# Optimization experiments

Hardware: AMD Instinct MI355X
Metric: run time of the kernel (lower is better)

## Reference

```python
import jax, jax.numpy as jnp
import numpy as np

DIM = 768
NUM_HEADS = 12
SCALE = 1.0 / (DIM ** 0.5)  # NOTE: source scales by 1/sqrt(dim), not 1/sqrt(head_dim)


def setup_inputs() -> dict:
    key = jax.random.key(0)
    k_x, k_qkv, k_ow, k_ob = jax.random.split(key, 4)
    b, n = 8, 1024
    x = jax.random.normal(k_x, (b, n, DIM), dtype=jnp.float32)
    # torch Linear weight is [out, in]; we store jax-style [in, out]
    w_qkv = jax.random.normal(k_qkv, (DIM, 3 * DIM), dtype=jnp.float32) * (DIM ** -0.5)
    w_out = jax.random.normal(k_ow, (DIM, DIM), dtype=jnp.float32) * (DIM ** -0.5)
    b_out = jax.random.normal(k_ob, (DIM,), dtype=jnp.float32) * 0.01
    return {"x": x, "w_qkv": w_qkv, "w_out": w_out, "b_out": b_out}


def reference(x, w_qkv, w_out, b_out):
    b, n, c = x.shape
    h = NUM_HEADS
    hd = c // h
    qkv = (x @ w_qkv).reshape(b, n, 3, h, hd)
    q, k, v = jnp.moveaxis(qkv, 2, 0)          # each [b, n, h, hd]
    q = jnp.swapaxes(q, 1, 2)                  # [b, h, n, hd]
    k = jnp.swapaxes(k, 1, 2)
    v = jnp.swapaxes(v, 1, 2)
    dot = jnp.einsum('bhqd,bhkd->bhqk', q, k) * SCALE
    attn = jax.nn.softmax(dot, axis=-1)        # attn_dropout p=0 -> identity
    out = jnp.einsum('bhqk,bhkd->bhqd', attn, v)
    out = jnp.swapaxes(out, 1, 2).reshape(b, n, c)
    return out @ w_out + b_out                 # proj_dropout p=0 -> identity
```

## Files before the change

### kernel.cpp

```cpp
#include <hip/hip_runtime.h>

#define DEV __device__ __forceinline__

typedef __bf16 bf16x8 __attribute__((ext_vector_type(8)));
typedef float  f32x4  __attribute__((ext_vector_type(4)));
typedef float  f32x16 __attribute__((ext_vector_type(16)));
typedef unsigned int u32x4 __attribute__((ext_vector_type(4)));

static constexpr float SCALE = 0.036084391824351615f;
static constexpr float L2E   = 1.4426950408889634f;

DEV unsigned short f2bf(float f) {
  return __builtin_bit_cast(unsigned short, (__bf16)f);
}
DEV unsigned int pack2(float a, float b) {
  return (unsigned int)f2bf(a) | ((unsigned int)f2bf(b) << 16);
}

#define GLDS16(gp, lp) \
  __builtin_amdgcn_global_load_lds((__attribute__((address_space(1))) void*)(gp), \
                                   (__attribute__((address_space(3))) void*)(lp), 16, 0, 0)


__global__ __launch_bounds__(256) void k_cvt_bf16(const float* __restrict__ in,
                                                  unsigned short* __restrict__ out,
                                                  int n8) {
  int i = blockIdx.x * 256 + threadIdx.x;
  if (i >= n8) return;
  const float4* p = (const float4*)in + (size_t)i * 2;
  float4 a = p[0], b = p[1];
  uint4 r;
  r.x = pack2(a.x, a.y); r.y = pack2(a.z, a.w);
  r.z = pack2(b.x, b.y); r.w = pack2(b.z, b.w);
  ((uint4*)out)[i] = r;
}

__global__ __launch_bounds__(256) void k_transpose_w(const float* __restrict__ in,
                                                     unsigned short* __restrict__ out,
                                                     int R, int C) {
  __shared__ float tile[64][65];
  int c0 = blockIdx.x * 64, r0 = blockIdx.y * 64;
  int t = threadIdx.x, tr = t >> 6, tc = t & 63;
#pragma unroll
  for (int i = 0; i < 64; i += 4)
    tile[i + tr][tc] = in[(size_t)(r0 + i + tr) * C + c0 + tc];
  __syncthreads();
#pragma unroll
  for (int i = 0; i < 64; i += 4)
    out[(size_t)(c0 + i + tr) * R + r0 + tc] = f2bf(tile[tc][i + tr]);
}

template <int MODE>
__global__ __launch_bounds__(256) void k_gemm(const unsigned short* __restrict__ A,
                                              const unsigned short* __restrict__ BT,
                                              void* __restrict__ out0,
                                              unsigned short* __restrict__ Kb,
                                              unsigned short* __restrict__ VTb,
                                              const float* __restrict__ bias) {
  __shared__ __align__(16) char smem[32768];
  char* As = smem;
  char* Bs = smem + 16384;
  const int tid = threadIdx.x;
  const int wave = tid >> 6, lane = tid & 63;
  const int g = lane >> 4, l15 = lane & 15;
  const int wrow = wave >> 1, wcol = wave & 1;

  int id = blockIdx.y * gridDim.x + blockIdx.x;
  int per_xcd = (gridDim.x * gridDim.y) >> 3;
  int id2 = (id & 7) * per_xcd + (id >> 3);
  const int bm = id2 / gridDim.x, bn = id2 % gridDim.x;

  f32x4 acc[4][4] = {};
  const unsigned short* Abase = A + (size_t)bm * 128 * 768;
  const unsigned short* Bbase = BT + (size_t)bn * 128 * 768;

  for (int kt = 0; kt < 12; ++kt) {
    const int k0 = kt * 64;
#pragma unroll
    for (int i = 0; i < 4; ++i) {
      int q = i * 256 + tid;
      int row = q >> 3, c = q & 7;
      int cs = c ^ (row & 7);
      GLDS16(Abase + (size_t)row * 768 + k0 + cs * 8, As + (i * 256 + wave * 64) * 16);
      GLDS16(Bbase + (size_t)row * 768 + k0 + cs * 8, Bs + (i * 256 + wave * 64) * 16);
    }
    __syncthreads();
    __builtin_amdgcn_s_setprio(1);
#pragma unroll
    for (int kk = 0; kk < 2; ++kk) {
      bf16x8 af[4], bfr[4];
#pragma unroll
      for (int mi = 0; mi < 4; ++mi) {
        int r = wrow * 64 + mi * 16 + l15;
        af[mi] = *(const bf16x8*)(As + r * 128 + (((kk * 4 + g) ^ (r & 7)) * 16));
      }
#pragma unroll
      for (int ni = 0; ni < 4; ++ni) {
        int r = wcol * 64 + ni * 16 + l15;
        bfr[ni] = *(const bf16x8*)(Bs + r * 128 + (((kk * 4 + g) ^ (r & 7)) * 16));
      }
#pragma unroll
      for (int mi = 0; mi < 4; ++mi)
#pragma unroll
        for (int ni = 0; ni < 4; ++ni)
          acc[mi][ni] = __builtin_amdgcn_mfma_f32_16x16x32_bf16(af[mi], bfr[ni], acc[mi][ni], 0, 0, 0);
    }
    __builtin_amdgcn_s_setprio(0);
    __syncthreads();
  }

  const int row0 = bm * 128 + wrow * 64;
  const int col0 = bn * 128 + wcol * 64;
#pragma unroll
  for (int mi = 0; mi < 4; ++mi) {
#pragma unroll
    for (int ni = 0; ni < 4; ++ni) {
      int col = col0 + ni * 16 + l15;
      if (MODE == 0) {
        int which = col / 768;
        int hd = col - which * 768;
        int head = hd >> 6, d = hd & 63;
        int rowm0 = row0 + mi * 16 + g * 4;
        int bi = rowm0 >> 10, np = rowm0 & 1023;
        if (which == 0) {
#pragma unroll
          for (int j = 0; j < 4; ++j)
            ((unsigned short*)out0)[((size_t)(bi * 12 + head) * 1024 + np + j) * 64 + d] =
                f2bf(acc[mi][ni][j] * (SCALE * L2E));
        } else if (which == 1) {
#pragma unroll
          for (int j = 0; j < 4; ++j)
            Kb[((size_t)(bi * 12 + head) * 1024 + np + j) * 64 + d] = f2bf(acc[mi][ni][j]);
        } else {
          ushort4 w;
          w.x = f2bf(acc[mi][ni][0]); w.y = f2bf(acc[mi][ni][1]);
          w.z = f2bf(acc[mi][ni][2]); w.w = f2bf(acc[mi][ni][3]);
          *(ushort4*)(VTb + ((size_t)(bi * 12 + head) * 64 + d) * 1024 + np) = w;
        }
      } else {
        float bz = bias[col];
#pragma unroll
        for (int j = 0; j < 4; ++j) {
          int rowm = row0 + mi * 16 + g * 4 + j;
          ((float*)out0)[(size_t)rowm * 768 + col] = acc[mi][ni][j] + bz;
        }
      }
    }
  }
}

__global__ __launch_bounds__(256) void k_attn(const unsigned short* __restrict__ Qb,
                                              const unsigned short* __restrict__ Kb,
                                              const unsigned short* __restrict__ VTb,
                                              unsigned short* __restrict__ Ao) {
  __shared__ __align__(16) char smem[32768];
  const int tid = threadIdx.x, wave = tid >> 6, lane = tid & 63;
  const int hi = lane >> 5, q31 = lane & 31;
  const int bh = blockIdx.x % 96, qt = blockIdx.x / 96;
  const int qbase = qt * 128 + wave * 32;
  const unsigned short* Kp = Kb + (size_t)bh * 65536;
  const unsigned short* Vp = VTb + (size_t)bh * 65536;

  auto STAGE = [&](int buf, int kt) {
#pragma unroll
    for (int i = 0; i < 2; ++i) {
      int c = i * 4 + wave;
      GLDS16(Kp + (size_t)(kt * 64 + lane) * 64 + c * 8,
             smem + buf * 8192 + (i * 256 + wave * 64) * 16);
      GLDS16(Vp + (size_t)lane * 1024 + kt * 64 + c * 8,
             smem + 16384 + buf * 8192 + (i * 256 + wave * 64) * 16);
    }
  };

  bf16x8 aq[4];
#pragma unroll
  for (int dk = 0; dk < 4; ++dk)
    aq[dk] = *(const bf16x8*)(Qb + (size_t)bh * 65536 +
                              (size_t)(qbase + q31) * 64 + dk * 16 + hi * 8);

  bf16x8 vones;
#pragma unroll
  for (int e = 0; e < 8; ++e) vones[e] = (__bf16)1.0f;

  f32x16 o0 = {}, o1 = {};
  f32x16 lacc = {};

  STAGE(0, 0);
  __syncthreads();
  int cur = 0;

  for (int kt = 0; kt < 16; ++kt) {
    if (kt < 15) STAGE(cur ^ 1, kt + 1);
    char* Ks = smem + cur * 8192;
    char* Vs = smem + 16384 + cur * 8192;

#pragma unroll
    for (int sub = 0; sub < 2; ++sub) {
      f32x16 st = {};
      __builtin_amdgcn_s_setprio(1);
#pragma unroll
      for (int dk = 0; dk < 4; ++dk) {
        bf16x8 ka = *(const bf16x8*)(Ks + (((dk * 2 + hi) * 64 + sub * 32 + q31) * 16));
        st = __builtin_amdgcn_mfma_f32_32x32x16_bf16(ka, aq[dk], st, 0, 0, 0);
      }
      __builtin_amdgcn_s_setprio(0);

      float ex[16];
#pragma unroll
      for (int r2 = 0; r2 < 16; ++r2) ex[r2] = __builtin_amdgcn_exp2f(st[r2]);

      unsigned w00 = pack2(ex[0], ex[1]),   w01 = pack2(ex[2], ex[3]);
      unsigned w10 = pack2(ex[4], ex[5]),   w11 = pack2(ex[6], ex[7]);
      unsigned w20 = pack2(ex[8], ex[9]),   w21 = pack2(ex[10], ex[11]);
      unsigned w30 = pack2(ex[12], ex[13]), w31 = pack2(ex[14], ex[15]);

      auto pA = __builtin_amdgcn_permlane32_swap(w00, w10, false, false);
      auto pB = __builtin_amdgcn_permlane32_swap(w01, w11, false, false);
      auto pC = __builtin_amdgcn_permlane32_swap(w20, w30, false, false);
      auto pD = __builtin_amdgcn_permlane32_swap(w21, w31, false, false);

      __builtin_amdgcn_s_setprio(1);
#pragma unroll
      for (int s = 0; s < 2; ++s) {
        u32x4 au;
        if (s == 0) { au[0] = pA[0]; au[1] = pB[0]; au[2] = pA[1]; au[3] = pB[1]; }
        else        { au[0] = pC[0]; au[1] = pD[0]; au[2] = pC[1]; au[3] = pD[1]; }
        bf16x8 pa = __builtin_bit_cast(bf16x8, au);
        int ch = sub * 4 + s * 2 + hi;
        bf16x8 vb0 = *(const bf16x8*)(Vs + (ch * 64 + q31) * 16);
        bf16x8 vb1 = *(const bf16x8*)(Vs + (ch * 64 + 32 + q31) * 16);
        o0   = __builtin_amdgcn_mfma_f32_32x32x16_bf16(pa, vb0, o0, 0, 0, 0);
        o1   = __builtin_amdgcn_mfma_f32_32x32x16_bf16(pa, vb1, o1, 0, 0, 0);
        lacc = __builtin_amdgcn_mfma_f32_32x32x16_bf16(pa, vones, lacc, 0, 0, 0);
      }
      __builtin_amdgcn_s_setprio(0);
    }

    __syncthreads();
    cur ^= 1;
  }

  const int b_idx = bh / 12, h = bh - b_idx * 12;
#pragma unroll
  for (int m = 0; m < 4; ++m) {
#pragma unroll
    for (int j = 0; j < 4; ++j) {
      int reg = m * 4 + j;
      int qr = j + 8 * m + 4 * hi;
      float linv = 1.0f / lacc[reg];
      size_t base = (size_t)(b_idx * 1024 + qbase + qr) * 768 + h * 64 + q31;
      Ao[base]      = f2bf(o0[reg] * linv);
      Ao[base + 32] = f2bf(o1[reg] * linv);
    }
  }
}


extern "C" void kernel_launch(void* const* d_in, const int* in_sizes, int n_in,
                              void* d_out, int out_size, void* d_ws, size_t ws_size,
                              hipStream_t stream) {
  const float* x     = (const float*)d_in[0];
  const float* w_qkv = (const float*)d_in[1];
  const float* w_out = (const float*)d_in[2];
  const float* b_out = (const float*)d_in[3];

  char* ws = (char*)d_ws;
  size_t off = 0;
  auto alloc = [&](size_t bytes) {
    void* p = ws + off;
    off += (bytes + 255) & ~(size_t)255;
    return p;
  };
  unsigned short* xb    = (unsigned short*)alloc(8192ull * 768 * 2);
  unsigned short* wqkvT = (unsigned short*)alloc(2304ull * 768 * 2);
  unsigned short* woutT = (unsigned short*)alloc(768ull * 768 * 2);
  unsigned short* Qb    = (unsigned short*)alloc(96ull * 1024 * 64 * 2);
  unsigned short* Kbf   = (unsigned short*)alloc(96ull * 1024 * 64 * 2);
  unsigned short* VTb   = (unsigned short*)alloc(96ull * 1024 * 64 * 2);
  unsigned short* Aob   = (unsigned short*)alloc(96ull * 1024 * 64 * 2);

  k_cvt_bf16<<<3072, 256, 0, stream>>>(x, xb, 786432);
  k_transpose_w<<<dim3(36, 12), 256, 0, stream>>>(w_qkv, wqkvT, 768, 2304);
  k_transpose_w<<<dim3(12, 12), 256, 0, stream>>>(w_out, woutT, 768, 768);
  k_gemm<0><<<dim3(18, 64), 256, 0, stream>>>(xb, wqkvT, Qb, Kbf, VTb, nullptr);
  k_attn<<<768, 256, 0, stream>>>(Qb, Kbf, VTb, Aob);
  k_gemm<1><<<dim3(6, 64), 256, 0, stream>>>(Aob, woutT, d_out, nullptr, nullptr, b_out);
}
```

Measured before the change: 110.4 us.

## Merge prep kernels into one launch and interleave QK MFMA sub-tiles in attention

Folds the x bf16 conversion and both weight transposes into a single k_prep launch, saving two kernel launches and their gaps. In the attention kernel, both 32-key QK^T score tiles are now computed together before the softmax/PV loop, so two independent MFMA chains can interleave. It also adds a minimum-occupancy hint of 3 blocks per CU via launch_bounds. The hint and the extra live accumulator registers may force spills or lower occupancy.

```diff
diff --git a/kernel.cpp b/kernel.cpp
--- a/kernel.cpp
+++ b/kernel.cpp
@@ -21,26 +21,36 @@
   __builtin_amdgcn_global_load_lds((__attribute__((address_space(1))) void*)(gp), \
                                    (__attribute__((address_space(3))) void*)(lp), 16, 0, 0)
 
-
-__global__ __launch_bounds__(256) void k_cvt_bf16(const float* __restrict__ in,
-                                                  unsigned short* __restrict__ out,
-                                                  int n8) {
-  int i = blockIdx.x * 256 + threadIdx.x;
-  if (i >= n8) return;
-  const float4* p = (const float4*)in + (size_t)i * 2;
-  float4 a = p[0], b = p[1];
-  uint4 r;
-  r.x = pack2(a.x, a.y); r.y = pack2(a.z, a.w);
-  r.z = pack2(b.x, b.y); r.w = pack2(b.z, b.w);
-  ((uint4*)out)[i] = r;
-}
-
-__global__ __launch_bounds__(256) void k_transpose_w(const float* __restrict__ in,
-                                                     unsigned short* __restrict__ out,
-                                                     int R, int C) {
+__global__ __launch_bounds__(256) void k_prep(const float* __restrict__ x,
+                                              const float* __restrict__ w_qkv,
+                                              const float* __restrict__ w_out,
+                                              unsigned short* __restrict__ xb,
+                                              unsigned short* __restrict__ wqkvT,
+                                              unsigned short* __restrict__ woutT) {
   __shared__ float tile[64][65];
-  int c0 = blockIdx.x * 64, r0 = blockIdx.y * 64;
-  int t = threadIdx.x, tr = t >> 6, tc = t & 63;
+  int b = blockIdx.x, t = threadIdx.x;
+  if (b < 3072) {
+    int i = b * 256 + t;
+    const float4* p = (const float4*)x + (size_t)i * 2;
+    float4 a = p[0], bb = p[1];
+    uint4 r;
+    r.x = pack2(a.x, a.y); r.y = pack2(a.z, a.w);
+    r.z = pack2(bb.x, bb.y); r.w = pack2(bb.z, bb.w);
+    ((uint4*)xb)[i] = r;
+    return;
+  }
+  const float* in;
+  unsigned short* out;
+  int R, C, bx, by;
+  if (b < 3504) {
+    int tt = b - 3072; in = w_qkv; out = wqkvT; R = 768; C = 2304;
+    bx = tt % 36; by = tt / 36;
+  } else {
+    int tt = b - 3504; in = w_out; out = woutT; R = 768; C = 768;
+    bx = tt % 12; by = tt / 12;
+  }
+  int c0 = bx * 64, r0 = by * 64;
+  int tr = t >> 6, tc = t & 63;
 #pragma unroll
   for (int i = 0; i < 64; i += 4)
     tile[i + tr][tc] = in[(size_t)(r0 + i + tr) * C + c0 + tc];
@@ -149,10 +159,10 @@
   }
 }
 
-__global__ __launch_bounds__(256) void k_attn(const unsigned short* __restrict__ Qb,
-                                              const unsigned short* __restrict__ Kb,
-                                              const unsigned short* __restrict__ VTb,
-                                              unsigned short* __restrict__ Ao) {
+__global__ __launch_bounds__(256, 3) void k_attn(const unsigned short* __restrict__ Qb,
+                                                 const unsigned short* __restrict__ Kb,
+                                                 const unsigned short* __restrict__ VTb,
+                                                 unsigned short* __restrict__ Ao) {
   __shared__ __align__(16) char smem[32768];
   const int tid = threadIdx.x, wave = tid >> 6, lane = tid & 63;
   const int hi = lane >> 5, q31 = lane & 31;
@@ -194,17 +204,20 @@
     char* Ks = smem + cur * 8192;
     char* Vs = smem + 16384 + cur * 8192;
 
+    f32x16 st0 = {}, st1 = {};
+    __builtin_amdgcn_s_setprio(1);
+#pragma unroll
+    for (int dk = 0; dk < 4; ++dk) {
+      bf16x8 ka0 = *(const bf16x8*)(Ks + (((dk * 2 + hi) * 64 + q31) * 16));
+      bf16x8 ka1 = *(const bf16x8*)(Ks + (((dk * 2 + hi) * 64 + 32 + q31) * 16));
+      st0 = __builtin_amdgcn_mfma_f32_32x32x16_bf16(ka0, aq[dk], st0, 0, 0, 0);
+      st1 = __builtin_amdgcn_mfma_f32_32x32x16_bf16(ka1, aq[dk], st1, 0, 0, 0);
+    }
+    __builtin_amdgcn_s_setprio(0);
+
 #pragma unroll
     for (int sub = 0; sub < 2; ++sub) {
-      f32x16 st = {};
-      __builtin_amdgcn_s_setprio(1);
-#pragma unroll
-      for (int dk = 0; dk < 4; ++dk) {
-        bf16x8 ka = *(const bf16x8*)(Ks + (((dk * 2 + hi) * 64 + sub * 32 + q31) * 16));
-        st = __builtin_amdgcn_mfma_f32_32x32x16_bf16(ka, aq[dk], st, 0, 0, 0);
-      }
-      __builtin_amdgcn_s_setprio(0);
-
+      const f32x16& st = sub ? st1 : st0;
       float ex[16];
 #pragma unroll
       for (int r2 = 0; r2 < 16; ++r2) ex[r2] = __builtin_amdgcn_exp2f(st[r2]);
@@ -279,9 +292,7 @@
   unsigned short* VTb   = (unsigned short*)alloc(96ull * 1024 * 64 * 2);
   unsigned short* Aob   = (unsigned short*)alloc(96ull * 1024 * 64 * 2);
 
-  k_cvt_bf16<<<3072, 256, 0, stream>>>(x, xb, 786432);
-  k_transpose_w<<<dim3(36, 12), 256, 0, stream>>>(w_qkv, wqkvT, 768, 2304);
-  k_transpose_w<<<dim3(12, 12), 256, 0, stream>>>(w_out, woutT, 768, 768);
+  k_prep<<<3648, 256, 0, stream>>>(x, w_qkv, w_out, xb, wqkvT, woutT);
   k_gemm<0><<<dim3(18, 64), 256, 0, stream>>>(xb, wqkvT, Qb, Kbf, VTb, nullptr);
   k_attn<<<768, 256, 0, stream>>>(Qb, Kbf, VTb, Aob);
   k_gemm<1><<<dim3(6, 64), 256, 0, stream>>>(Aob, woutT, d_out, nullptr, nullptr, b_out);
```

New measurement: 103.9 us. 5.9% less time.
